# Kernel tuning notes

Measured on AMD Instinct MI355X. Metric: run time of the kernel, lower is better.

The kernel has to match this reference:

```python
import jax, jax.numpy as jnp
import numpy as np

D = 8           # spatial size of conv feature map
K = 24          # conv channels
Q = 128         # question embedding size
IN_SIZE = 2 * (K + 2) + Q  # 180
HID = 256
OUT = 28


def _coords(d):
    # faithful to torch float-tensor arithmetic: a/d is float division
    a = jnp.arange(d * d, dtype=jnp.float32)
    cx = (a / d - d / 2) / (d / 2.0)
    cy = (a % d - d / 2) / (d / 2.0)
    return jnp.stack([cx, cy], axis=1)  # [d^2, 2]


def setup_inputs() -> dict:
    key = jax.random.key(0)
    ks = jax.random.split(key, 16)
    s = 0.05
    inp = {
        "x": jax.random.normal(ks[0], (64, K, D, D), dtype=jnp.float32),
        "qst": jax.random.normal(ks[1], (64, Q), dtype=jnp.float32),
        # g MLP (weights stored [in, out])
        "g1_w": jax.random.normal(ks[2], (IN_SIZE, HID), dtype=jnp.float32) * s,
        "g1_b": jnp.zeros((HID,), dtype=jnp.float32),
        "g2_w": jax.random.normal(ks[3], (HID, HID), dtype=jnp.float32) * s,
        "g2_b": jnp.zeros((HID,), dtype=jnp.float32),
        "g3_w": jax.random.normal(ks[4], (HID, HID), dtype=jnp.float32) * s,
        "g3_b": jnp.zeros((HID,), dtype=jnp.float32),
        "g4_w": jax.random.normal(ks[5], (HID, HID), dtype=jnp.float32) * s,
        "g4_b": jnp.zeros((HID,), dtype=jnp.float32),
        # f MLP
        "f1_w": jax.random.normal(ks[6], (HID, HID), dtype=jnp.float32) * s,
        "f1_b": jnp.zeros((HID,), dtype=jnp.float32),
        "f2_w": jax.random.normal(ks[7], (HID, HID), dtype=jnp.float32) * s,
        "f2_b": jnp.zeros((HID,), dtype=jnp.float32),
        "f3_w": jax.random.normal(ks[8], (HID, OUT), dtype=jnp.float32) * s,
        "f3_b": jnp.zeros((OUT,), dtype=jnp.float32),
    }
    return inp


def _forward(x, qst, g1_w, g1_b, g2_w, g2_b, g3_w, g3_b, g4_w, g4_b,
             f1_w, f1_b, f2_w, f2_b, f3_w, f3_b):
    b, k, d, _ = x.shape
    n = d * d  # 64 objects
    # [b, n, k] object features + 2 coord channels -> [b, n, 26]
    xf = jnp.transpose(x.reshape(b, k, n), (0, 2, 1))
    ct = jnp.broadcast_to(_coords(d)[None], (b, n, 2))
    xf = jnp.concatenate([xf, ct], axis=2)                      # [b, n, 26]
    obj = k + 2
    # x_i: varies along axis 2 (original torch layout); x_j varies along axis 1 and carries qst
    xi = jnp.broadcast_to(xf[:, None, :, :], (b, n, n, obj))
    xjq = jnp.concatenate(
        [xf, jnp.broadcast_to(qst[:, None, :], (b, n, qst.shape[1]))], axis=2)
    xj = jnp.broadcast_to(xjq[:, :, None, :], (b, n, n, obj + qst.shape[1]))
    pair = jnp.concatenate([xi, xj], axis=3)                    # [b, n, n, 180]
    # g MLP over all pairs
    h = jax.nn.relu(pair @ g1_w + g1_b)
    h = jax.nn.relu(h @ g2_w + g2_b)
    h = jax.nn.relu(h @ g3_w + g3_b)
    h = jax.nn.relu(h @ g4_w + g4_b)                            # [b, n, n, 256]
    xg = jnp.sum(h, axis=(1, 2))                                # sum over d^4 pairs
    # f MLP (dropout is identity in eval mode)
    xf_ = jax.nn.relu(xg @ f1_w + f1_b)
    xf_ = jax.nn.relu(xf_ @ f2_w + f2_b)
    logits = xf_ @ f3_w + f3_b
    return jax.nn.log_softmax(logits, axis=-1)


def reference(x, qst, g1_w, g1_b, g2_w, g2_b, g3_w, g3_b, g4_w, g4_b,
              f1_w, f1_b, f2_w, f2_b, f3_w, f3_b):
    return _forward(x, qst, g1_w, g1_b, g2_w, g2_b, g3_w, g3_b, g4_w, g4_b,
                    f1_w, f1_b, f2_w, f2_b, f3_w, f3_b)
```

## Files before the change

### kernel.cpp

```cpp
#include <hip/hip_runtime.h>

typedef __bf16 bf16_t;
typedef __bf16 bf16x8 __attribute__((ext_vector_type(8)));
typedef __bf16 bf16x4 __attribute__((ext_vector_type(4)));
typedef float  f32x4  __attribute__((ext_vector_type(4)));


__global__ __launch_bounds__(256) void rn_prep_kernel(
    const float* __restrict__ x, const float* __restrict__ qst,
    const float* __restrict__ g1w, const float* __restrict__ g1b,
    const float* __restrict__ g2w, const float* __restrict__ g3w,
    const float* __restrict__ g4w,
    float* __restrict__ A, float* __restrict__ C,
    bf16_t* __restrict__ Wt, float* __restrict__ xg)
{
  __shared__ float T[64][65];
  int blk = blockIdx.x;
  int n   = threadIdx.x;
  if (blk < 256) {
    int b  = blk >> 2;
    int jg = (blk & 3) * 16;
    float accQ = g1b[n];
    const float* qb = qst + b * 128;
    #pragma unroll 8
    for (int qi = 0; qi < 128; ++qi)
      accQ += qb[qi] * g1w[(52 + qi) * 256 + n];

    float w24 = g1w[24 * 256 + n], w25 = g1w[25 * 256 + n];
    float w50 = g1w[50 * 256 + n], w51 = g1w[51 * 256 + n];
    float accA[16], accC[16];
    #pragma unroll
    for (int t = 0; t < 16; ++t) {
      int j = jg + t;
      float cx = ((float)j * 0.125f - 4.0f) * 0.25f;
      float cy = ((float)(j & 7) - 4.0f) * 0.25f;
      accA[t] = cx * w24 + cy * w25;
      accC[t] = accQ + cx * w50 + cy * w51;
    }
    for (int c = 0; c < 24; ++c) {
      float wa = g1w[c * 256 + n];
      float wc = g1w[(26 + c) * 256 + n];
      const float* xc = x + (b * 24 + c) * 64 + jg;
      #pragma unroll
      for (int t = 0; t < 16; ++t) {
        float xv = xc[t];
        accA[t] += xv * wa;
        accC[t] += xv * wc;
      }
    }
    #pragma unroll
    for (int t = 0; t < 16; ++t) {
      A[(b * 64 + jg + t) * 256 + n] = accA[t];
      C[(b * 64 + jg + t) * 256 + n] = accC[t];
    }
  } else if (blk < 256 + 48) {
    int t   = blk - 256;
    int mat = t >> 4;
    int tl  = t & 15;
    int kt  = (tl & 3) * 64;
    int nt_ = (tl >> 2) * 64;
    const float* W = (mat == 0) ? g2w : (mat == 1 ? g3w : g4w);
    int lane = n & 63, w = n >> 6;
    #pragma unroll
    for (int it = 0; it < 16; ++it) {
      int kl = w * 16 + it;
      T[kl][lane] = W[(kt + kl) * 256 + nt_ + lane];
    }
    __syncthreads();
    #pragma unroll
    for (int it = 0; it < 16; ++it) {
      int nl  = w * 16 + it;
      int no  = nt_ + nl;
      int k   = kt + lane;
      int tile = no >> 4, rr = no & 15;
      int ksI  = k >> 5,  qI = (k >> 3) & 3, e = k & 7;
      int idx  = ((tile * 8 + ksI) * 64 + qI * 16 + rr) * 8 + e;
      Wt[mat * 65536 + idx] = (bf16_t)T[lane][nl];
    }
  } else {
    int idx = (blk - (256 + 48)) * 256 + n;
    xg[idx] = 0.f;
  }
}

__global__ __launch_bounds__(256, 2) void rn_main_kernel(
    const float* __restrict__ A, const float* __restrict__ C,
    const bf16_t* __restrict__ Wt,
    const float* __restrict__ g2b, const float* __restrict__ g3b,
    const float* __restrict__ g4b,
    float* __restrict__ xg)
{
  __shared__ bf16_t h0[16384];
  __shared__ bf16_t h1[16384];

  int tid  = threadIdx.x;
  int bx0  = blockIdx.x;
  int bx   = (bx0 & 7) * 256 + (bx0 >> 3);
  int b    = bx >> 5;
  int ip   = bx & 31;
  int lane = tid & 63;
  int wave = tid >> 6;
  int r    = lane & 15;
  int q    = lane >> 4;

  {
    const float* Ab = A + (size_t)b * 64 * 256;
    const float* Cr = C + ((size_t)b * 64 + ip * 2) * 256;
    int j = wave * 16 + r;
    #pragma unroll
    for (int it = 0; it < 8; ++it) {
      int k0 = it * 32 + q * 8;
      const float4 a0  = *(const float4*)(Ab + j * 256 + k0);
      const float4 a1  = *(const float4*)(Ab + j * 256 + k0 + 4);
      const float4 c00 = *(const float4*)(Cr + k0);
      const float4 c01 = *(const float4*)(Cr + k0 + 4);
      const float4 c10 = *(const float4*)(Cr + 256 + k0);
      const float4 c11 = *(const float4*)(Cr + 256 + k0 + 4);
      bf16x8 v0, v1;
      v0[0] = (bf16_t)fmaxf(a0.x + c00.x, 0.f);
      v0[1] = (bf16_t)fmaxf(a0.y + c00.y, 0.f);
      v0[2] = (bf16_t)fmaxf(a0.z + c00.z, 0.f);
      v0[3] = (bf16_t)fmaxf(a0.w + c00.w, 0.f);
      v0[4] = (bf16_t)fmaxf(a1.x + c01.x, 0.f);
      v0[5] = (bf16_t)fmaxf(a1.y + c01.y, 0.f);
      v0[6] = (bf16_t)fmaxf(a1.z + c01.z, 0.f);
      v0[7] = (bf16_t)fmaxf(a1.w + c01.w, 0.f);
      v1[0] = (bf16_t)fmaxf(a0.x + c10.x, 0.f);
      v1[1] = (bf16_t)fmaxf(a0.y + c10.y, 0.f);
      v1[2] = (bf16_t)fmaxf(a0.z + c10.z, 0.f);
      v1[3] = (bf16_t)fmaxf(a0.w + c10.w, 0.f);
      v1[4] = (bf16_t)fmaxf(a1.x + c11.x, 0.f);
      v1[5] = (bf16_t)fmaxf(a1.y + c11.y, 0.f);
      v1[6] = (bf16_t)fmaxf(a1.z + c11.z, 0.f);
      v1[7] = (bf16_t)fmaxf(a1.w + c11.w, 0.f);
      int off = ((wave * 8 + it) * 64 + lane) * 8;
      *(bf16x8*)&h0[off] = v0;
      *(bf16x8*)&h1[off] = v1;
    }
  }

  for (int L = 0; L < 3; ++L) {
    __syncthreads();
    const bf16_t* Wl   = Wt + L * 65536 + wave * 16384;
    const float*  bias = (L == 0) ? g2b : (L == 1) ? g3b : g4b;

    f32x4 acc[4][8];
    #pragma unroll
    for (int nt = 0; nt < 4; ++nt)
      #pragma unroll
      for (int mt = 0; mt < 8; ++mt)
        #pragma unroll
        for (int e = 0; e < 4; ++e) acc[nt][mt][e] = 0.f;

    #pragma unroll
    for (int ks = 0; ks < 8; ++ks) {
      bf16x8 wf[4], hf[8];
      #pragma unroll
      for (int nt = 0; nt < 4; ++nt)
        wf[nt] = *(const bf16x8*)&Wl[((nt * 8 + ks) * 64 + lane) * 8];
      #pragma unroll
      for (int mt = 0; mt < 8; ++mt) {
        const bf16_t* hb = (mt < 4) ? h0 : h1;
        hf[mt] = *(const bf16x8*)&hb[(((mt & 3) * 8 + ks) * 64 + lane) * 8];
      }
      #pragma unroll
      for (int nt = 0; nt < 4; ++nt)
        #pragma unroll
        for (int mt = 0; mt < 8; ++mt)
          acc[nt][mt] = __builtin_amdgcn_mfma_f32_16x16x32_bf16(
              wf[nt], hf[mt], acc[nt][mt], 0, 0, 0);
    }

    __syncthreads();

    if (L < 2) {
      #pragma unroll
      for (int nt = 0; nt < 4; ++nt) {
        int k0  = wave * 64 + nt * 16 + q * 4;
        float4 bv = *(const float4*)&bias[k0];
        int ks_ = k0 >> 5, rem = k0 & 31;
        int qp  = rem >> 3, e0 = rem & 7;
        #pragma unroll
        for (int mt = 0; mt < 8; ++mt) {
          bf16_t* hb = (mt < 4) ? h0 : h1;
          bf16x4 v;
          v[0] = (bf16_t)fmaxf(acc[nt][mt][0] + bv.x, 0.f);
          v[1] = (bf16_t)fmaxf(acc[nt][mt][1] + bv.y, 0.f);
          v[2] = (bf16_t)fmaxf(acc[nt][mt][2] + bv.z, 0.f);
          v[3] = (bf16_t)fmaxf(acc[nt][mt][3] + bv.w, 0.f);
          int off = (((mt & 3) * 8 + ks_) * 64 + qp * 16 + r) * 8 + e0;
          *(bf16x4*)&hb[off] = v;
        }
      }
    } else {
      #pragma unroll
      for (int nt = 0; nt < 4; ++nt) {
        int k0 = wave * 64 + nt * 16 + q * 4;
        float4 bv = *(const float4*)&bias[k0];
        float p0 = 0.f, p1 = 0.f, p2 = 0.f, p3 = 0.f;
        #pragma unroll
        for (int mt = 0; mt < 8; ++mt) {
          p0 += fmaxf(acc[nt][mt][0] + bv.x, 0.f);
          p1 += fmaxf(acc[nt][mt][1] + bv.y, 0.f);
          p2 += fmaxf(acc[nt][mt][2] + bv.z, 0.f);
          p3 += fmaxf(acc[nt][mt][3] + bv.w, 0.f);
        }
        #pragma unroll
        for (int d = 1; d < 16; d <<= 1) {
          p0 += __shfl_xor(p0, d, 64);
          p1 += __shfl_xor(p1, d, 64);
          p2 += __shfl_xor(p2, d, 64);
          p3 += __shfl_xor(p3, d, 64);
        }
        if (r == 0) {
          int nn = b * 256 + k0;
          atomicAdd(&xg[nn + 0], p0);
          atomicAdd(&xg[nn + 1], p1);
          atomicAdd(&xg[nn + 2], p2);
          atomicAdd(&xg[nn + 3], p3);
        }
      }
    }
  }
}

__global__ __launch_bounds__(256) void rn_f_kernel(
    const float* __restrict__ xg,
    const float* __restrict__ f1w, const float* __restrict__ f1b,
    const float* __restrict__ f2w, const float* __restrict__ f2b,
    const float* __restrict__ f3w, const float* __restrict__ f3b,
    float* __restrict__ out)
{
  __shared__ float xs[256], t1[256], t2[256], lg[28], lse[1];
  int b = blockIdx.x, tid = threadIdx.x;
  xs[tid] = xg[b * 256 + tid];
  __syncthreads();
  float acc = f1b[tid];
  for (int k = 0; k < 256; ++k) acc += xs[k] * f1w[k * 256 + tid];
  t1[tid] = fmaxf(acc, 0.f);
  __syncthreads();
  acc = f2b[tid];
  for (int k = 0; k < 256; ++k) acc += t1[k] * f2w[k * 256 + tid];
  t2[tid] = fmaxf(acc, 0.f);
  __syncthreads();
  if (tid < 28) {
    float a2 = f3b[tid];
    for (int k = 0; k < 256; ++k) a2 += t2[k] * f3w[k * 28 + tid];
    lg[tid] = a2;
  }
  __syncthreads();
  if (tid == 0) {
    float m = lg[0];
    for (int j = 1; j < 28; ++j) m = fmaxf(m, lg[j]);
    float se = 0.f;
    for (int j = 0; j < 28; ++j) se += expf(lg[j] - m);
    lse[0] = m + logf(se);
  }
  __syncthreads();
  if (tid < 28) out[b * 28 + tid] = lg[tid] - lse[0];
}

extern "C" void kernel_launch(void* const* d_in, const int* in_sizes, int n_in,
                              void* d_out, int out_size, void* d_ws, size_t ws_size,
                              hipStream_t stream) {
  (void)in_sizes; (void)n_in; (void)out_size; (void)ws_size;
  const float* x   = (const float*)d_in[0];
  const float* qst = (const float*)d_in[1];
  const float* g1w = (const float*)d_in[2];
  const float* g1b = (const float*)d_in[3];
  const float* g2w = (const float*)d_in[4];
  const float* g2b = (const float*)d_in[5];
  const float* g3w = (const float*)d_in[6];
  const float* g3b = (const float*)d_in[7];
  const float* g4w = (const float*)d_in[8];
  const float* g4b = (const float*)d_in[9];
  const float* f1w = (const float*)d_in[10];
  const float* f1b = (const float*)d_in[11];
  const float* f2w = (const float*)d_in[12];
  const float* f2b = (const float*)d_in[13];
  const float* f3w = (const float*)d_in[14];
  const float* f3b = (const float*)d_in[15];
  float* out = (float*)d_out;

  float*  A  = (float*)d_ws;
  float*  C  = A + 4096 * 256;
  bf16_t* Wt = (bf16_t*)(C + 4096 * 256);
  float*  xg = (float*)((char*)Wt + 3 * 65536 * sizeof(bf16_t));

  rn_prep_kernel<<<256 + 48 + 64, 256, 0, stream>>>(
      x, qst, g1w, g1b, g2w, g3w, g4w, A, C, Wt, xg);
  rn_main_kernel<<<2048, 256, 0, stream>>>(A, C, Wt, g2b, g3b, g4b, xg);
  rn_f_kernel<<<64, 256, 0, stream>>>(xg, f1w, f1b, f2w, f2b, f3w, f3b, out);
}
```

Measured before the change: 246.2 us.

## Halve per-block pair tile and replace atomics with per-block partial sums

The main kernel now processes one i-row (64 pairs) per block instead of two. That halves the LDS buffer and the accumulator registers, raises the launch-bounds occupancy hint from 2 to 4 blocks, and doubles the grid to 4096 blocks. The final-layer atomicAdds are replaced by writes of per-block partial vectors, which the f-kernel sums over 64 rows, so the xg zeroing in the prep kernel is dropped. The trade-off is that each weight fragment loaded from global is reused over half as many MFMAs, so weight traffic per pair doubles.

```diff
diff --git a/kernel.cpp b/kernel.cpp
--- a/kernel.cpp
+++ b/kernel.cpp
@@ -12,7 +12,7 @@
     const float* __restrict__ g2w, const float* __restrict__ g3w,
     const float* __restrict__ g4w,
     float* __restrict__ A, float* __restrict__ C,
-    bf16_t* __restrict__ Wt, float* __restrict__ xg)
+    bf16_t* __restrict__ Wt)
 {
   __shared__ float T[64][65];
   int blk = blockIdx.x;
@@ -53,7 +53,7 @@
       A[(b * 64 + jg + t) * 256 + n] = accA[t];
       C[(b * 64 + jg + t) * 256 + n] = accC[t];
     }
-  } else if (blk < 256 + 48) {
+  } else {
     int t   = blk - 256;
     int mat = t >> 4;
     int tl  = t & 15;
@@ -77,27 +77,23 @@
       int idx  = ((tile * 8 + ksI) * 64 + qI * 16 + rr) * 8 + e;
       Wt[mat * 65536 + idx] = (bf16_t)T[lane][nl];
     }
-  } else {
-    int idx = (blk - (256 + 48)) * 256 + n;
-    xg[idx] = 0.f;
-  }
-}
-
-__global__ __launch_bounds__(256, 2) void rn_main_kernel(
+  }
+}
+
+__global__ __launch_bounds__(256, 4) void rn_main_kernel(
     const float* __restrict__ A, const float* __restrict__ C,
     const bf16_t* __restrict__ Wt,
     const float* __restrict__ g2b, const float* __restrict__ g3b,
     const float* __restrict__ g4b,
-    float* __restrict__ xg)
+    float* __restrict__ part)
 {
-  __shared__ bf16_t h0[16384];
-  __shared__ bf16_t h1[16384];
+  __shared__ bf16_t h[16384];
 
   int tid  = threadIdx.x;
   int bx0  = blockIdx.x;
-  int bx   = (bx0 & 7) * 256 + (bx0 >> 3);
-  int b    = bx >> 5;
-  int ip   = bx & 31;
+  int bx   = (bx0 & 7) * 512 + (bx0 >> 3);
+  int b    = bx >> 6;
+  int i    = bx & 63;
   int lane = tid & 63;
   int wave = tid >> 6;
   int r    = lane & 15;
@@ -105,37 +101,25 @@
 
   {
     const float* Ab = A + (size_t)b * 64 * 256;
-    const float* Cr = C + ((size_t)b * 64 + ip * 2) * 256;
+    const float* Cr = C + ((size_t)b * 64 + i) * 256;
     int j = wave * 16 + r;
     #pragma unroll
     for (int it = 0; it < 8; ++it) {
       int k0 = it * 32 + q * 8;
-      const float4 a0  = *(const float4*)(Ab + j * 256 + k0);
-      const float4 a1  = *(const float4*)(Ab + j * 256 + k0 + 4);
-      const float4 c00 = *(const float4*)(Cr + k0);
-      const float4 c01 = *(const float4*)(Cr + k0 + 4);
-      const float4 c10 = *(const float4*)(Cr + 256 + k0);
-      const float4 c11 = *(const float4*)(Cr + 256 + k0 + 4);
-      bf16x8 v0, v1;
-      v0[0] = (bf16_t)fmaxf(a0.x + c00.x, 0.f);
-      v0[1] = (bf16_t)fmaxf(a0.y + c00.y, 0.f);
-      v0[2] = (bf16_t)fmaxf(a0.z + c00.z, 0.f);
-      v0[3] = (bf16_t)fmaxf(a0.w + c00.w, 0.f);
-      v0[4] = (bf16_t)fmaxf(a1.x + c01.x, 0.f);
-      v0[5] = (bf16_t)fmaxf(a1.y + c01.y, 0.f);
-      v0[6] = (bf16_t)fmaxf(a1.z + c01.z, 0.f);
-      v0[7] = (bf16_t)fmaxf(a1.w + c01.w, 0.f);
-      v1[0] = (bf16_t)fmaxf(a0.x + c10.x, 0.f);
-      v1[1] = (bf16_t)fmaxf(a0.y + c10.y, 0.f);
-      v1[2] = (bf16_t)fmaxf(a0.z + c10.z, 0.f);
-      v1[3] = (bf16_t)fmaxf(a0.w + c10.w, 0.f);
-      v1[4] = (bf16_t)fmaxf(a1.x + c11.x, 0.f);
-      v1[5] = (bf16_t)fmaxf(a1.y + c11.y, 0.f);
-      v1[6] = (bf16_t)fmaxf(a1.z + c11.z, 0.f);
-      v1[7] = (bf16_t)fmaxf(a1.w + c11.w, 0.f);
-      int off = ((wave * 8 + it) * 64 + lane) * 8;
-      *(bf16x8*)&h0[off] = v0;
-      *(bf16x8*)&h1[off] = v1;
+      const float4 a0 = *(const float4*)(Ab + j * 256 + k0);
+      const float4 a1 = *(const float4*)(Ab + j * 256 + k0 + 4);
+      const float4 c0 = *(const float4*)(Cr + k0);
+      const float4 c1 = *(const float4*)(Cr + k0 + 4);
+      bf16x8 v;
+      v[0] = (bf16_t)fmaxf(a0.x + c0.x, 0.f);
+      v[1] = (bf16_t)fmaxf(a0.y + c0.y, 0.f);
+      v[2] = (bf16_t)fmaxf(a0.z + c0.z, 0.f);
+      v[3] = (bf16_t)fmaxf(a0.w + c0.w, 0.f);
+      v[4] = (bf16_t)fmaxf(a1.x + c1.x, 0.f);
+      v[5] = (bf16_t)fmaxf(a1.y + c1.y, 0.f);
+      v[6] = (bf16_t)fmaxf(a1.z + c1.z, 0.f);
+      v[7] = (bf16_t)fmaxf(a1.w + c1.w, 0.f);
+      *(bf16x8*)&h[((wave * 8 + it) * 64 + lane) * 8] = v;
     }
   }
 
@@ -144,29 +128,27 @@
     const bf16_t* Wl   = Wt + L * 65536 + wave * 16384;
     const float*  bias = (L == 0) ? g2b : (L == 1) ? g3b : g4b;
 
-    f32x4 acc[4][8];
+    f32x4 acc[4][4];
     #pragma unroll
     for (int nt = 0; nt < 4; ++nt)
       #pragma unroll
-      for (int mt = 0; mt < 8; ++mt)
+      for (int mt = 0; mt < 4; ++mt)
         #pragma unroll
         for (int e = 0; e < 4; ++e) acc[nt][mt][e] = 0.f;
 
     #pragma unroll
     for (int ks = 0; ks < 8; ++ks) {
-      bf16x8 wf[4], hf[8];
+      bf16x8 wf[4], hf[4];
       #pragma unroll
       for (int nt = 0; nt < 4; ++nt)
         wf[nt] = *(const bf16x8*)&Wl[((nt * 8 + ks) * 64 + lane) * 8];
       #pragma unroll
-      for (int mt = 0; mt < 8; ++mt) {
-        const bf16_t* hb = (mt < 4) ? h0 : h1;
-        hf[mt] = *(const bf16x8*)&hb[(((mt & 3) * 8 + ks) * 64 + lane) * 8];
-      }
+      for (int mt = 0; mt < 4; ++mt)
+        hf[mt] = *(const bf16x8*)&h[((mt * 8 + ks) * 64 + lane) * 8];
       #pragma unroll
       for (int nt = 0; nt < 4; ++nt)
         #pragma unroll
-        for (int mt = 0; mt < 8; ++mt)
+        for (int mt = 0; mt < 4; ++mt)
           acc[nt][mt] = __builtin_amdgcn_mfma_f32_16x16x32_bf16(
               wf[nt], hf[mt], acc[nt][mt], 0, 0, 0);
     }
@@ -181,15 +163,14 @@
         int ks_ = k0 >> 5, rem = k0 & 31;
         int qp  = rem >> 3, e0 = rem & 7;
         #pragma unroll
-        for (int mt = 0; mt < 8; ++mt) {
-          bf16_t* hb = (mt < 4) ? h0 : h1;
+        for (int mt = 0; mt < 4; ++mt) {
           bf16x4 v;
           v[0] = (bf16_t)fmaxf(acc[nt][mt][0] + bv.x, 0.f);
           v[1] = (bf16_t)fmaxf(acc[nt][mt][1] + bv.y, 0.f);
           v[2] = (bf16_t)fmaxf(acc[nt][mt][2] + bv.z, 0.f);
           v[3] = (bf16_t)fmaxf(acc[nt][mt][3] + bv.w, 0.f);
-          int off = (((mt & 3) * 8 + ks_) * 64 + qp * 16 + r) * 8 + e0;
-          *(bf16x4*)&hb[off] = v;
+          int off = ((mt * 8 + ks_) * 64 + qp * 16 + r) * 8 + e0;
+          *(bf16x4*)&h[off] = v;
         }
       }
     } else {
@@ -199,7 +180,7 @@
         float4 bv = *(const float4*)&bias[k0];
         float p0 = 0.f, p1 = 0.f, p2 = 0.f, p3 = 0.f;
         #pragma unroll
-        for (int mt = 0; mt < 8; ++mt) {
+        for (int mt = 0; mt < 4; ++mt) {
           p0 += fmaxf(acc[nt][mt][0] + bv.x, 0.f);
           p1 += fmaxf(acc[nt][mt][1] + bv.y, 0.f);
           p2 += fmaxf(acc[nt][mt][2] + bv.z, 0.f);
@@ -213,11 +194,8 @@
           p3 += __shfl_xor(p3, d, 64);
         }
         if (r == 0) {
-          int nn = b * 256 + k0;
-          atomicAdd(&xg[nn + 0], p0);
-          atomicAdd(&xg[nn + 1], p1);
-          atomicAdd(&xg[nn + 2], p2);
-          atomicAdd(&xg[nn + 3], p3);
+          float4 pv = make_float4(p0, p1, p2, p3);
+          *(float4*)&part[(size_t)bx * 256 + k0] = pv;
         }
       }
     }
@@ -225,7 +203,7 @@
 }
 
 __global__ __launch_bounds__(256) void rn_f_kernel(
-    const float* __restrict__ xg,
+    const float* __restrict__ part,
     const float* __restrict__ f1w, const float* __restrict__ f1b,
     const float* __restrict__ f2w, const float* __restrict__ f2b,
     const float* __restrict__ f3w, const float* __restrict__ f3b,
@@ -233,7 +211,11 @@
 {
   __shared__ float xs[256], t1[256], t2[256], lg[28], lse[1];
   int b = blockIdx.x, tid = threadIdx.x;
-  xs[tid] = xg[b * 256 + tid];
+  float s = 0.f;
+  const float* pb = part + (size_t)b * 64 * 256;
+  #pragma unroll 8
+  for (int i = 0; i < 64; ++i) s += pb[i * 256 + tid];
+  xs[tid] = s;
   __syncthreads();
   float acc = f1b[tid];
   for (int k = 0; k < 256; ++k) acc += xs[k] * f1w[k * 256 + tid];
@@ -282,13 +264,13 @@
   const float* f3b = (const float*)d_in[15];
   float* out = (float*)d_out;
 
-  float*  A  = (float*)d_ws;
-  float*  C  = A + 4096 * 256;
-  bf16_t* Wt = (bf16_t*)(C + 4096 * 256);
-  float*  xg = (float*)((char*)Wt + 3 * 65536 * sizeof(bf16_t));
-
-  rn_prep_kernel<<<256 + 48 + 64, 256, 0, stream>>>(
-      x, qst, g1w, g1b, g2w, g3w, g4w, A, C, Wt, xg);
-  rn_main_kernel<<<2048, 256, 0, stream>>>(A, C, Wt, g2b, g3b, g4b, xg);
-  rn_f_kernel<<<64, 256, 0, stream>>>(xg, f1w, f1b, f2w, f2b, f3w, f3b, out);
-}
+  float*  A    = (float*)d_ws;
+  float*  C    = A + 4096 * 256;
+  bf16_t* Wt   = (bf16_t*)(C + 4096 * 256);
+  float*  part = (float*)((char*)Wt + 3 * 65536 * sizeof(bf16_t));
+
+  rn_prep_kernel<<<256 + 48, 256, 0, stream>>>(
+      x, qst, g1w, g1b, g2w, g3w, g4w, A, C, Wt);
+  rn_main_kernel<<<4096, 256, 0, stream>>>(A, C, Wt, g2b, g3b, g4b, part);
+  rn_f_kernel<<<64, 256, 0, stream>>>(part, f1w, f1b, f2w, f2b, f3w, f3b, out);
+}
```

New measurement: 252.3 us. +2.5%, slower.

## Preload layer weights into registers and replace atomics with partial-sum buffer

Applied to the files above, without the earlier changes.

The main kernel now loads all of each wave's weight fragments for a layer into registers before the barrier, so the MFMA loop no longer issues global weight loads inside the k-loop. Launch bounds drop to one block per SIMD set, making room for the larger register footprint. The final-layer atomicAdds into xg are replaced by per-block float4 stores into a partial buffer, which the f kernel reduces over 32 entries per batch, so the zeroing blocks in the prep kernel are removed. The cost is higher register pressure, possibly lower occupancy, and a larger workspace write.

```diff
diff --git a/kernel.cpp b/kernel.cpp
--- a/kernel.cpp
+++ b/kernel.cpp
@@ -12,7 +12,7 @@
     const float* __restrict__ g2w, const float* __restrict__ g3w,
     const float* __restrict__ g4w,
     float* __restrict__ A, float* __restrict__ C,
-    bf16_t* __restrict__ Wt, float* __restrict__ xg)
+    bf16_t* __restrict__ Wt)
 {
   __shared__ float T[64][65];
   int blk = blockIdx.x;
@@ -53,7 +53,7 @@
       A[(b * 64 + jg + t) * 256 + n] = accA[t];
       C[(b * 64 + jg + t) * 256 + n] = accC[t];
     }
-  } else if (blk < 256 + 48) {
+  } else {
     int t   = blk - 256;
     int mat = t >> 4;
     int tl  = t & 15;
@@ -77,18 +77,15 @@
       int idx  = ((tile * 8 + ksI) * 64 + qI * 16 + rr) * 8 + e;
       Wt[mat * 65536 + idx] = (bf16_t)T[lane][nl];
     }
-  } else {
-    int idx = (blk - (256 + 48)) * 256 + n;
-    xg[idx] = 0.f;
-  }
-}
-
-__global__ __launch_bounds__(256, 2) void rn_main_kernel(
+  }
+}
+
+__global__ __launch_bounds__(256, 1) void rn_main_kernel(
     const float* __restrict__ A, const float* __restrict__ C,
     const bf16_t* __restrict__ Wt,
     const float* __restrict__ g2b, const float* __restrict__ g3b,
     const float* __restrict__ g4b,
-    float* __restrict__ xg)
+    float* __restrict__ part)
 {
   __shared__ bf16_t h0[16384];
   __shared__ bf16_t h1[16384];
@@ -140,9 +137,17 @@
   }
 
   for (int L = 0; L < 3; ++L) {
+    const bf16_t* Wl = Wt + L * 65536 + wave * 16384;
+    bf16x8 wreg[4][8];
+    #pragma unroll
+    for (int nt = 0; nt < 4; ++nt)
+      #pragma unroll
+      for (int ks = 0; ks < 8; ++ks)
+        wreg[nt][ks] = *(const bf16x8*)&Wl[((nt * 8 + ks) * 64 + lane) * 8];
+
+    const float* bias = (L == 0) ? g2b : (L == 1) ? g3b : g4b;
+
     __syncthreads();
-    const bf16_t* Wl   = Wt + L * 65536 + wave * 16384;
-    const float*  bias = (L == 0) ? g2b : (L == 1) ? g3b : g4b;
 
     f32x4 acc[4][8];
     #pragma unroll
@@ -154,10 +159,7 @@
 
     #pragma unroll
     for (int ks = 0; ks < 8; ++ks) {
-      bf16x8 wf[4], hf[8];
-      #pragma unroll
-      for (int nt = 0; nt < 4; ++nt)
-        wf[nt] = *(const bf16x8*)&Wl[((nt * 8 + ks) * 64 + lane) * 8];
+      bf16x8 hf[8];
       #pragma unroll
       for (int mt = 0; mt < 8; ++mt) {
         const bf16_t* hb = (mt < 4) ? h0 : h1;
@@ -168,7 +170,7 @@
         #pragma unroll
         for (int mt = 0; mt < 8; ++mt)
           acc[nt][mt] = __builtin_amdgcn_mfma_f32_16x16x32_bf16(
-              wf[nt], hf[mt], acc[nt][mt], 0, 0, 0);
+              wreg[nt][ks], hf[mt], acc[nt][mt], 0, 0, 0);
     }
 
     __syncthreads();
@@ -213,11 +215,8 @@
           p3 += __shfl_xor(p3, d, 64);
         }
         if (r == 0) {
-          int nn = b * 256 + k0;
-          atomicAdd(&xg[nn + 0], p0);
-          atomicAdd(&xg[nn + 1], p1);
-          atomicAdd(&xg[nn + 2], p2);
-          atomicAdd(&xg[nn + 3], p3);
+          float4 pv = make_float4(p0, p1, p2, p3);
+          *(float4*)&part[(size_t)bx * 256 + k0] = pv;
         }
       }
     }
@@ -225,7 +224,7 @@
 }
 
 __global__ __launch_bounds__(256) void rn_f_kernel(
-    const float* __restrict__ xg,
+    const float* __restrict__ part,
     const float* __restrict__ f1w, const float* __restrict__ f1b,
     const float* __restrict__ f2w, const float* __restrict__ f2b,
     const float* __restrict__ f3w, const float* __restrict__ f3b,
@@ -233,7 +232,11 @@
 {
   __shared__ float xs[256], t1[256], t2[256], lg[28], lse[1];
   int b = blockIdx.x, tid = threadIdx.x;
-  xs[tid] = xg[b * 256 + tid];
+  float s = 0.f;
+  const float* pb = part + (size_t)b * 32 * 256;
+  #pragma unroll 8
+  for (int i = 0; i < 32; ++i) s += pb[i * 256 + tid];
+  xs[tid] = s;
   __syncthreads();
   float acc = f1b[tid];
   for (int k = 0; k < 256; ++k) acc += xs[k] * f1w[k * 256 + tid];
@@ -282,13 +285,13 @@
   const float* f3b = (const float*)d_in[15];
   float* out = (float*)d_out;
 
-  float*  A  = (float*)d_ws;
-  float*  C  = A + 4096 * 256;
-  bf16_t* Wt = (bf16_t*)(C + 4096 * 256);
-  float*  xg = (float*)((char*)Wt + 3 * 65536 * sizeof(bf16_t));
-
-  rn_prep_kernel<<<256 + 48 + 64, 256, 0, stream>>>(
-      x, qst, g1w, g1b, g2w, g3w, g4w, A, C, Wt, xg);
-  rn_main_kernel<<<2048, 256, 0, stream>>>(A, C, Wt, g2b, g3b, g4b, xg);
-  rn_f_kernel<<<64, 256, 0, stream>>>(xg, f1w, f1b, f2w, f2b, f3w, f3b, out);
-}
+  float*  A    = (float*)d_ws;
+  float*  C    = A + 4096 * 256;
+  bf16_t* Wt   = (bf16_t*)(C + 4096 * 256);
+  float*  part = (float*)((char*)Wt + 3 * 65536 * sizeof(bf16_t));
+
+  rn_prep_kernel<<<256 + 48, 256, 0, stream>>>(
+      x, qst, g1w, g1b, g2w, g3w, g4w, A, C, Wt);
+  rn_main_kernel<<<2048, 256, 0, stream>>>(A, C, Wt, g2b, g3b, g4b, part);
+  rn_f_kernel<<<64, 256, 0, stream>>>(part, f1w, f1b, f2w, f2b, f3w, f3b, out);
+}
```

Measured after the change: 251.3 us. 1.02x slower.
